# Optimization experiments

Measured on AMD Instinct MI355X. Metric: run time of the kernel, lower is better.

The kernel has to match this reference:

```python
import jax, jax.numpy as jnp
import numpy as np

E = 1024
H = 16
D = E // H  # head dim 64


def setup_inputs() -> dict:
    key = jax.random.key(0)
    ks = jax.random.split(key, 8)
    B, S = 4, 2048
    scale = 1.0 / np.sqrt(E)
    return {
        "Q": jax.random.normal(ks[0], (B, S, E), jnp.float32),
        "K": jax.random.normal(ks[1], (B, S, E), jnp.float32),
        "V": jax.random.normal(ks[2], (B, S, E), jnp.float32),
        "Wq": jax.random.normal(ks[3], (E, E), jnp.float32) * scale,
        "Wk": jax.random.normal(ks[4], (E, E), jnp.float32) * scale,
        "Wv": jax.random.normal(ks[5], (E, E), jnp.float32) * scale,
        "Wo": jax.random.normal(ks[6], (E, E), jnp.float32) * scale,
        "bo": jax.random.normal(ks[7], (E,), jnp.float32) * 0.01,
    }


def _split_heads(x):
    # [B, S, E] -> [B, H, S, D]
    B, S, _ = x.shape
    return x.reshape(B, S, H, D).transpose(0, 2, 1, 3)


def reference(Q, K, V, Wq, Wk, Wv, Wo, bo):
    # Linear (torch nn.Linear: x @ W.T), no bias for QKV
    q = _split_heads(Q @ Wq.T)  # [B,H,Sq,D]
    k = _split_heads(K @ Wk.T)  # [B,H,Sk,D]
    v = _split_heads(V @ Wv.T)  # [B,H,Sk,D]
    scores = jnp.einsum("bhqd,bhkd->bhqk", q, k)
    # NOTE: original code computes scores/sqrt(D) but applies softmax to the
    # UNSCALED scores (a bug we reproduce faithfully).
    attn = jax.nn.softmax(scores, axis=-1)
    out = jnp.einsum("bhqk,bhkd->bhqd", attn, v)  # [B,H,Sq,D]
    B, _, Sq, _ = out.shape
    out = out.transpose(0, 2, 1, 3).reshape(B, Sq, E)
    return out @ Wo.T + bo
```

## Files before the change

### kernel.cpp

```cpp
#include <hip/hip_runtime.h>
#include <hip/hip_bf16.h>


using bf16 = __hip_bfloat16;
typedef __attribute__((ext_vector_type(8))) short short8;
typedef __attribute__((ext_vector_type(4))) short short4v;
typedef _Float16 half8 __attribute__((ext_vector_type(8)));
typedef __attribute__((ext_vector_type(4))) float floatx4;

#define E_DIM 1024
#define H_NUM 16
#define D_DIM 64
#define B_NUM 4
#define S_LEN 2048
#define M_TOT 8192

__device__ __forceinline__ void async_ld16(const void* g, void* l) {
  __builtin_amdgcn_global_load_lds(
      (const __attribute__((address_space(1))) unsigned int*)g,
      (__attribute__((address_space(3))) unsigned int*)l, 16, 0, 0);
}

__device__ __forceinline__ short f2bf(float x) {
  unsigned u = __builtin_bit_cast(unsigned, x);
  u += 0x7FFFu + ((u >> 16) & 1u);
  return (short)(u >> 16);
}

__global__ void cvt_f32_bf16(const float* __restrict__ src,
                             short* __restrict__ dst, int n4) {
  int i = blockIdx.x * blockDim.x + threadIdx.x;
  if (i >= n4) return;
  float4 v = ((const float4*)src)[i];
  short4v o;
  o[0] = f2bf(v.x); o[1] = f2bf(v.y); o[2] = f2bf(v.z); o[3] = f2bf(v.w);
  ((short4v*)dst)[i] = o;
}

template <int OUT_MODE>
__global__ __launch_bounds__(256, 3) void gemm_k(
    const short* __restrict__ A, const short* __restrict__ Wb,
    const float* __restrict__ bias, void* __restrict__ Cp,
    int M, int N, int K) {
  __shared__ __align__(16) short As[128 * 32];
  __shared__ __align__(16) short Ws[128 * 32];
  const int tid = threadIdx.x;
  const int wave = tid >> 6;
  const int lane = tid & 63;
  const int quad = lane >> 4;
  const int l16 = lane & 15;
  const int wr = wave >> 1, wc = wave & 1;

  int mBase, nBase;
  {
    const int nwg = gridDim.x * gridDim.y;
    int l = blockIdx.x + gridDim.x * blockIdx.y;
    l = (l & 7) * (nwg >> 3) + (l >> 3);
    nBase = (l & 7) * 128;
    mBase = (l >> 3) * 128;
  }

  floatx4 acc[4][4] = {};

  const int sR = lane >> 2, sC = (lane & 3) * 8;
  for (int kb = 0; kb < K; kb += 32) {
    __syncthreads();
#pragma unroll
    for (int t = 0; t < 2; t++) {
      const int r0 = wave * 32 + t * 16;
      async_ld16(&Wb[(size_t)(nBase + r0 + sR) * K + kb + sC], &Ws[r0 * 32]);
    }
#pragma unroll
    for (int t = 0; t < 2; t++) {
      const int r0 = wave * 32 + t * 16;
      async_ld16(&A[(size_t)(mBase + r0 + sR) * K + kb + sC], &As[r0 * 32]);
    }
    __syncthreads();

    short8 af[4], wf[4];
#pragma unroll
    for (int i = 0; i < 4; i++)
      af[i] = *(const short8*)&As[(wr * 64 + i * 16 + l16) * 32 + quad * 8];
#pragma unroll
    for (int j = 0; j < 4; j++)
      wf[j] = *(const short8*)&Ws[(wc * 64 + j * 16 + l16) * 32 + quad * 8];
#pragma unroll
    for (int i = 0; i < 4; i++)
#pragma unroll
      for (int j = 0; j < 4; j++)
        acc[i][j] = __builtin_amdgcn_mfma_f32_16x16x32_bf16(af[i], wf[j], acc[i][j], 0, 0, 0);
  }

#pragma unroll
  for (int i = 0; i < 4; i++) {
    const int row0 = mBase + wr * 64 + i * 16 + quad * 4;
#pragma unroll
    for (int j = 0; j < 4; j++) {
      const int col = nBase + wc * 64 + j * 16 + l16;
      const float bv = (OUT_MODE == 2) ? bias[col] : 0.0f;
#pragma unroll
      for (int r = 0; r < 4; r++) {
        const float val = acc[i][j][r] + bv;
        if (OUT_MODE == 0)
          ((_Float16*)Cp)[(size_t)(row0 + r) * N + col] = (_Float16)val;
        else if (OUT_MODE == 1)
          ((short*)Cp)[(size_t)col * M + (row0 + r)] = f2bf(val);
        else
          ((float*)Cp)[(size_t)(row0 + r) * N + col] = val;
      }
    }
  }
}

__global__ __launch_bounds__(256, 3) void flash_attn(
    const _Float16* __restrict__ q, const _Float16* __restrict__ k,
    const short* __restrict__ vt, short* __restrict__ o) {
  __shared__ __align__(16) char smem[51200];
  short* Vts = (short*)smem;
  _Float16* Ks = (_Float16*)(smem + 16384);
  short* PsW = (short*)(smem + 16384 + (threadIdx.x >> 6) * 8704);

  const int tid = threadIdx.x;
  const int wave = tid >> 6;
  const int lane = tid & 63;
  const int quad = lane >> 4;
  const int l16 = lane & 15;

  int qRow0, h, b;
  {
    int l = blockIdx.x + ((blockIdx.y + (blockIdx.z << 4)) << 4);
    l = (l & 7) * 128 + (l >> 3);
    qRow0 = (l & 15) * 128;
    h = (l >> 4) & 15;
    b = l >> 8;
  }

  const _Float16* qp = q + (size_t)(b * S_LEN + qRow0) * E_DIM + h * D_DIM;
  const _Float16* kp = k + (size_t)(b * S_LEN) * E_DIM + h * D_DIM;
  const short* vtp = vt + (size_t)(h * D_DIM) * M_TOT + b * S_LEN;
  short* op = o + (size_t)(b * S_LEN + qRow0) * E_DIM + h * D_DIM;

  half8 qf[2][2];
#pragma unroll
  for (int i = 0; i < 2; i++)
#pragma unroll
    for (int ks = 0; ks < 2; ks++)
      qf[i][ks] = *(const half8*)&qp[(size_t)(wave * 32 + i * 16 + l16) * E_DIM + ks * 32 + quad * 8];

  short8 ones;
#pragma unroll
  for (int j = 0; j < 8; j++) ones[j] = (l16 == 0) ? (short)0x3F80 : (short)0;

  floatx4 oacc[2][4] = {};
  floatx4 oaccL[2] = {};

  const int kRow = lane >> 3, kChk = lane & 7;
  const int vRow = lane >> 4, vChk = lane & 15;

  for (int kt = 0; kt < 16; kt++) {
    __syncthreads();
#pragma unroll
    for (int t = 0; t < 4; t++) {
      const int r0 = wave * 32 + t * 8;
      const int gcol = (kChk ^ kRow) * 8;
      async_ld16(&kp[(size_t)(kt * 128 + r0 + kRow) * E_DIM + gcol], &Ks[r0 * 64]);
    }
#pragma unroll
    for (int t = 0; t < 4; t++) {
      const int r0 = wave * 16 + t * 4;
      const int row = r0 + vRow;
      const int gcol = (vChk ^ (row & 15)) * 8;
      async_ld16(&vtp[(size_t)row * M_TOT + kt * 128 + gcol], &Vts[r0 * 128]);
    }
    __syncthreads();

    floatx4 sc[2][8] = {};
    __builtin_amdgcn_s_setprio(1);
#pragma unroll
    for (int jt = 0; jt < 8; jt++) {
#pragma unroll
      for (int ks = 0; ks < 2; ks++) {
        const int scol = ((ks * 4 + quad) ^ (l16 & 7)) * 8;
        half8 kf = *(const half8*)&Ks[(jt * 16 + l16) * 64 + scol];
        sc[0][jt] = __builtin_amdgcn_mfma_f32_16x16x32_f16(qf[0][ks], kf, sc[0][jt], 0, 0, 0);
        sc[1][jt] = __builtin_amdgcn_mfma_f32_16x16x32_f16(qf[1][ks], kf, sc[1][jt], 0, 0, 0);
      }
    }
    __builtin_amdgcn_s_setprio(0);
    __syncthreads();

#pragma unroll
    for (int i = 0; i < 2; i++)
#pragma unroll
      for (int r = 0; r < 4; r++) {
        const int prow = i * 16 + quad * 4 + r;
#pragma unroll
        for (int jt = 0; jt < 8; jt++) {
          const float p = __expf(sc[i][jt][r] - 40.0f);
          PsW[prow * 136 + jt * 16 + l16] = f2bf(p);
        }
      }

    __builtin_amdgcn_s_setprio(1);
#pragma unroll
    for (int ks = 0; ks < 4; ks++) {
      short8 pf[2];
#pragma unroll
      for (int i = 0; i < 2; i++)
        pf[i] = *(const short8*)&PsW[(i * 16 + l16) * 136 + ks * 32 + quad * 8];
#pragma unroll
      for (int dt = 0; dt < 4; dt++) {
        const int scol = ((ks * 4 + quad) ^ l16) * 8;
        short8 vf = *(const short8*)&Vts[(dt * 16 + l16) * 128 + scol];
        oacc[0][dt] = __builtin_amdgcn_mfma_f32_16x16x32_bf16(pf[0], vf, oacc[0][dt], 0, 0, 0);
        oacc[1][dt] = __builtin_amdgcn_mfma_f32_16x16x32_bf16(pf[1], vf, oacc[1][dt], 0, 0, 0);
      }
      oaccL[0] = __builtin_amdgcn_mfma_f32_16x16x32_bf16(pf[0], ones, oaccL[0], 0, 0, 0);
      oaccL[1] = __builtin_amdgcn_mfma_f32_16x16x32_bf16(pf[1], ones, oaccL[1], 0, 0, 0);
    }
    __builtin_amdgcn_s_setprio(0);
  }

#pragma unroll
  for (int i = 0; i < 2; i++)
#pragma unroll
    for (int r = 0; r < 4; r++) {
      const float ls = __shfl(oaccL[i][r], lane & 48, 64);
      const float inv = 1.0f / ls;
      const int row = wave * 32 + i * 16 + quad * 4 + r;
#pragma unroll
      for (int dt = 0; dt < 4; dt++)
        op[(size_t)row * E_DIM + dt * 16 + l16] = f2bf(oacc[i][dt][r] * inv);
    }
}

extern "C" void kernel_launch(void* const* d_in, const int* in_sizes, int n_in,
                              void* d_out, int out_size, void* d_ws, size_t ws_size,
                              hipStream_t stream) {
  const float* Q  = (const float*)d_in[0];
  const float* K  = (const float*)d_in[1];
  const float* V  = (const float*)d_in[2];
  const float* Wq = (const float*)d_in[3];
  const float* Wk = (const float*)d_in[4];
  const float* Wv = (const float*)d_in[5];
  const float* Wo = (const float*)d_in[6];
  const float* bo = (const float*)d_in[7];
  float* out = (float*)d_out;

  char* ws = (char*)d_ws;
  const size_t wsz = (size_t)E_DIM * E_DIM * 2;
  short* wqb = (short*)ws; ws += wsz;
  short* wkb = (short*)ws; ws += wsz;
  short* wvb = (short*)ws; ws += wsz;
  short* wob = (short*)ws; ws += wsz;
  const size_t asz = (size_t)M_TOT * E_DIM * 2;
  _Float16* qw = (_Float16*)ws; ws += asz;
  _Float16* kw = (_Float16*)ws; ws += asz;
  short* vtw = (short*)ws;      ws += asz;
  short* aw  = (short*)ws;      ws += asz;
  short* abf = aw;

  dim3 blk(256);
  const int n4w = E_DIM * E_DIM / 4;
  cvt_f32_bf16<<<dim3(n4w / 256), blk, 0, stream>>>(Wq, wqb, n4w);
  cvt_f32_bf16<<<dim3(n4w / 256), blk, 0, stream>>>(Wk, wkb, n4w);
  cvt_f32_bf16<<<dim3(n4w / 256), blk, 0, stream>>>(Wv, wvb, n4w);
  cvt_f32_bf16<<<dim3(n4w / 256), blk, 0, stream>>>(Wo, wob, n4w);

  const int n4a = M_TOT * E_DIM / 4;
  dim3 ggrid(E_DIM / 128, M_TOT / 128);
  cvt_f32_bf16<<<dim3(n4a / 256), blk, 0, stream>>>(Q, abf, n4a);
  gemm_k<0><<<ggrid, blk, 0, stream>>>(abf, wqb, nullptr, qw, M_TOT, E_DIM, E_DIM);
  cvt_f32_bf16<<<dim3(n4a / 256), blk, 0, stream>>>(K, abf, n4a);
  gemm_k<0><<<ggrid, blk, 0, stream>>>(abf, wkb, nullptr, kw, M_TOT, E_DIM, E_DIM);
  cvt_f32_bf16<<<dim3(n4a / 256), blk, 0, stream>>>(V, abf, n4a);
  gemm_k<1><<<ggrid, blk, 0, stream>>>(abf, wvb, nullptr, vtw, M_TOT, E_DIM, E_DIM);
  flash_attn<<<dim3(S_LEN / 128, H_NUM, B_NUM), blk, 0, stream>>>(qw, kw, vtw, aw);
  gemm_k<2><<<ggrid, blk, 0, stream>>>(aw, wob, bo, out, M_TOT, E_DIM, E_DIM);
}
```

Measured before the change: 376.3 us.

## Batch QKV projections into one launch with swizzled BK64 tiles and LDS-staged transpose

Merges the four weight conversions and the three activation conversions into two batched kernels. The Q/K/V projections now run as a single grid-z batched GEMM, reusing the output buffer as scratch for the bf16 K and V copies. The GEMM now uses a K-step of 64 with an XOR-swizzled LDS layout to cut bank conflicts and halve barrier count. The transposed V output is staged through LDS so it can be written with coalesced 16-byte stores instead of strided scalar stores. This removes launch gaps and uncoalesced writes, at the cost of more LDS per block and a different block-to-tile mapping.

```diff
diff --git a/kernel.cpp b/kernel.cpp
--- a/kernel.cpp
+++ b/kernel.cpp
@@ -27,23 +27,46 @@
   return (short)(u >> 16);
 }
 
-__global__ void cvt_f32_bf16(const float* __restrict__ src,
-                             short* __restrict__ dst, int n4) {
-  int i = blockIdx.x * blockDim.x + threadIdx.x;
-  if (i >= n4) return;
+__global__ void cvt_w4(const float* __restrict__ a, const float* __restrict__ b,
+                       const float* __restrict__ c, const float* __restrict__ d,
+                       short* __restrict__ oa, short* __restrict__ ob,
+                       short* __restrict__ oc, short* __restrict__ od) {
+  const int z = blockIdx.y;
+  const float* src = z == 0 ? a : z == 1 ? b : z == 2 ? c : d;
+  short* dst = z == 0 ? oa : z == 1 ? ob : z == 2 ? oc : od;
+  const int i = blockIdx.x * blockDim.x + threadIdx.x;
   float4 v = ((const float4*)src)[i];
   short4v o;
   o[0] = f2bf(v.x); o[1] = f2bf(v.y); o[2] = f2bf(v.z); o[3] = f2bf(v.w);
   ((short4v*)dst)[i] = o;
 }
 
-template <int OUT_MODE>
+__global__ void cvt_a3(const float* __restrict__ a, const float* __restrict__ b,
+                       const float* __restrict__ c, short* __restrict__ oa,
+                       short* __restrict__ ob, short* __restrict__ oc) {
+  const int z = blockIdx.y;
+  const float* src = z == 0 ? a : z == 1 ? b : c;
+  short* dst = z == 0 ? oa : z == 1 ? ob : oc;
+  const int i = blockIdx.x * blockDim.x + threadIdx.x;
+  float4 v = ((const float4*)src)[i];
+  short4v o;
+  o[0] = f2bf(v.x); o[1] = f2bf(v.y); o[2] = f2bf(v.z); o[3] = f2bf(v.w);
+  ((short4v*)dst)[i] = o;
+}
+
+template <int MODE>
 __global__ __launch_bounds__(256, 3) void gemm_k(
-    const short* __restrict__ A, const short* __restrict__ Wb,
-    const float* __restrict__ bias, void* __restrict__ Cp,
-    int M, int N, int K) {
-  __shared__ __align__(16) short As[128 * 32];
-  __shared__ __align__(16) short Ws[128 * 32];
+    const short* __restrict__ A0, const short* __restrict__ A1,
+    const short* __restrict__ A2, const short* __restrict__ W0,
+    const short* __restrict__ W1, const short* __restrict__ W2,
+    void* __restrict__ C0, void* __restrict__ C1p, void* __restrict__ C2p,
+    const float* __restrict__ bias) {
+  __shared__ __align__(16) char smem[MODE == 0 ? 34816 : 32768];
+  short* As = (short*)smem;
+  short* Ws = (short*)(smem + 16384);
+  short* Cs = (short*)smem;
+
+  const int M = M_TOT, N = E_DIM, K = E_DIM;
   const int tid = threadIdx.x;
   const int wave = tid >> 6;
   const int lane = tid & 63;
@@ -51,63 +74,94 @@
   const int l16 = lane & 15;
   const int wr = wave >> 1, wc = wave & 1;
 
-  int mBase, nBase;
-  {
-    const int nwg = gridDim.x * gridDim.y;
-    int l = blockIdx.x + gridDim.x * blockIdx.y;
-    l = (l & 7) * (nwg >> 3) + (l >> 3);
-    nBase = (l & 7) * 128;
-    mBase = (l >> 3) * 128;
+  const int z = (MODE == 0) ? blockIdx.z : 0;
+  const short* A = (MODE == 0) ? (z == 0 ? A0 : z == 1 ? A1 : A2) : A0;
+  const short* W = (MODE == 0) ? (z == 0 ? W0 : z == 1 ? W1 : W2) : W0;
+
+  const int nBase = (blockIdx.y & 7) * 128;
+  const int mBase = (blockIdx.x * 8 + (blockIdx.y >> 3)) * 128;
+
+  const int sRow = lane >> 3;
+  const int sSwz = ((lane & 7) ^ sRow) * 8;
+  const int rdSwz0 = ((0 * 4 + quad) ^ (l16 & 7)) * 8;
+  const int rdSwz1 = ((1 * 4 + quad) ^ (l16 & 7)) * 8;
+
+  floatx4 acc[4][4] = {};
+
+  for (int kb = 0; kb < K; kb += 64) {
+    __syncthreads();
+#pragma unroll
+    for (int t = 0; t < 4; t++) {
+      const int r0 = wave * 32 + t * 8;
+      async_ld16(&W[(size_t)(nBase + r0 + sRow) * K + kb + sSwz], &Ws[r0 * 64]);
+      async_ld16(&A[(size_t)(mBase + r0 + sRow) * K + kb + sSwz], &As[r0 * 64]);
+    }
+    __syncthreads();
+#pragma unroll
+    for (int ks = 0; ks < 2; ks++) {
+      const int rs = ks ? rdSwz1 : rdSwz0;
+      short8 af[4], wf[4];
+#pragma unroll
+      for (int i = 0; i < 4; i++)
+        af[i] = *(const short8*)&As[(wr * 64 + i * 16 + l16) * 64 + rs];
+#pragma unroll
+      for (int j = 0; j < 4; j++)
+        wf[j] = *(const short8*)&Ws[(wc * 64 + j * 16 + l16) * 64 + rs];
+#pragma unroll
+      for (int i = 0; i < 4; i++)
+#pragma unroll
+        for (int j = 0; j < 4; j++)
+          acc[i][j] = __builtin_amdgcn_mfma_f32_16x16x32_bf16(af[i], wf[j], acc[i][j], 0, 0, 0);
+    }
   }
 
-  floatx4 acc[4][4] = {};
-
-  const int sR = lane >> 2, sC = (lane & 3) * 8;
-  for (int kb = 0; kb < K; kb += 32) {
-    __syncthreads();
-#pragma unroll
-    for (int t = 0; t < 2; t++) {
-      const int r0 = wave * 32 + t * 16;
-      async_ld16(&Wb[(size_t)(nBase + r0 + sR) * K + kb + sC], &Ws[r0 * 32]);
-    }
-#pragma unroll
-    for (int t = 0; t < 2; t++) {
-      const int r0 = wave * 32 + t * 16;
-      async_ld16(&A[(size_t)(mBase + r0 + sR) * K + kb + sC], &As[r0 * 32]);
-    }
-    __syncthreads();
-
-    short8 af[4], wf[4];
-#pragma unroll
-    for (int i = 0; i < 4; i++)
-      af[i] = *(const short8*)&As[(wr * 64 + i * 16 + l16) * 32 + quad * 8];
-#pragma unroll
-    for (int j = 0; j < 4; j++)
-      wf[j] = *(const short8*)&Ws[(wc * 64 + j * 16 + l16) * 32 + quad * 8];
-#pragma unroll
-    for (int i = 0; i < 4; i++)
-#pragma unroll
-      for (int j = 0; j < 4; j++)
-        acc[i][j] = __builtin_amdgcn_mfma_f32_16x16x32_bf16(af[i], wf[j], acc[i][j], 0, 0, 0);
-  }
-
-#pragma unroll
-  for (int i = 0; i < 4; i++) {
-    const int row0 = mBase + wr * 64 + i * 16 + quad * 4;
-#pragma unroll
-    for (int j = 0; j < 4; j++) {
-      const int col = nBase + wc * 64 + j * 16 + l16;
-      const float bv = (OUT_MODE == 2) ? bias[col] : 0.0f;
-#pragma unroll
-      for (int r = 0; r < 4; r++) {
-        const float val = acc[i][j][r] + bv;
-        if (OUT_MODE == 0)
-          ((_Float16*)Cp)[(size_t)(row0 + r) * N + col] = (_Float16)val;
-        else if (OUT_MODE == 1)
-          ((short*)Cp)[(size_t)col * M + (row0 + r)] = f2bf(val);
-        else
-          ((float*)Cp)[(size_t)(row0 + r) * N + col] = val;
-      }
+  if (MODE == 2) {
+#pragma unroll
+    for (int i = 0; i < 4; i++) {
+      const int row0 = mBase + wr * 64 + i * 16 + quad * 4;
+#pragma unroll
+      for (int j = 0; j < 4; j++) {
+        const int col = nBase + wc * 64 + j * 16 + l16;
+        const float bv = bias[col];
+#pragma unroll
+        for (int r = 0; r < 4; r++)
+          ((float*)C0)[(size_t)(row0 + r) * N + col] = acc[i][j][r] + bv;
+      }
+    }
+  } else if (z != 2) {
+    _Float16* C = (_Float16*)(z == 0 ? C0 : C1p);
+#pragma unroll
+    for (int i = 0; i < 4; i++) {
+      const int row0 = mBase + wr * 64 + i * 16 + quad * 4;
+#pragma unroll
+      for (int j = 0; j < 4; j++) {
+        const int col = nBase + wc * 64 + j * 16 + l16;
+#pragma unroll
+        for (int r = 0; r < 4; r++)
+          C[(size_t)(row0 + r) * N + col] = (_Float16)acc[i][j][r];
+      }
+    }
+  } else {
+    __syncthreads();
+#pragma unroll
+    for (int i = 0; i < 4; i++) {
+      const int rl = wr * 64 + i * 16 + quad * 4;
+#pragma unroll
+      for (int j = 0; j < 4; j++) {
+        const int cl = wc * 64 + j * 16 + l16;
+#pragma unroll
+        for (int r = 0; r < 4; r++)
+          Cs[cl * 136 + rl + r] = f2bf(acc[i][j][r]);
+      }
+    }
+    __syncthreads();
+    short* C = (short*)C2p;
+#pragma unroll
+    for (int p = 0; p < 8; p++) {
+      const int id = p * 256 + tid;
+      const int nl = id >> 4, mc = (id & 15) * 8;
+      *(short8*)&C[(size_t)(nBase + nl) * M + mBase + mc] =
+          *(const short8*)&Cs[nl * 136 + mc];
     }
   }
 }
@@ -258,23 +312,19 @@
   _Float16* kw = (_Float16*)ws; ws += asz;
   short* vtw = (short*)ws;      ws += asz;
   short* aw  = (short*)ws;      ws += asz;
-  short* abf = aw;
+  short* qbf = aw;
+  short* kbf = (short*)d_out;
+  short* vbf = (short*)d_out + (size_t)M_TOT * E_DIM;
 
   dim3 blk(256);
-  const int n4w = E_DIM * E_DIM / 4;
-  cvt_f32_bf16<<<dim3(n4w / 256), blk, 0, stream>>>(Wq, wqb, n4w);
-  cvt_f32_bf16<<<dim3(n4w / 256), blk, 0, stream>>>(Wk, wkb, n4w);
-  cvt_f32_bf16<<<dim3(n4w / 256), blk, 0, stream>>>(Wv, wvb, n4w);
-  cvt_f32_bf16<<<dim3(n4w / 256), blk, 0, stream>>>(Wo, wob, n4w);
-
-  const int n4a = M_TOT * E_DIM / 4;
-  dim3 ggrid(E_DIM / 128, M_TOT / 128);
-  cvt_f32_bf16<<<dim3(n4a / 256), blk, 0, stream>>>(Q, abf, n4a);
-  gemm_k<0><<<ggrid, blk, 0, stream>>>(abf, wqb, nullptr, qw, M_TOT, E_DIM, E_DIM);
-  cvt_f32_bf16<<<dim3(n4a / 256), blk, 0, stream>>>(K, abf, n4a);
-  gemm_k<0><<<ggrid, blk, 0, stream>>>(abf, wkb, nullptr, kw, M_TOT, E_DIM, E_DIM);
-  cvt_f32_bf16<<<dim3(n4a / 256), blk, 0, stream>>>(V, abf, n4a);
-  gemm_k<1><<<ggrid, blk, 0, stream>>>(abf, wvb, nullptr, vtw, M_TOT, E_DIM, E_DIM);
+  cvt_w4<<<dim3(E_DIM * E_DIM / 4 / 256, 4), blk, 0, stream>>>(
+      Wq, Wk, Wv, Wo, wqb, wkb, wvb, wob);
+  cvt_a3<<<dim3(M_TOT * E_DIM / 4 / 256, 3), blk, 0, stream>>>(
+      Q, K, V, qbf, kbf, vbf);
+
+  gemm_k<0><<<dim3(8, 64, 3), blk, 0, stream>>>(
+      qbf, kbf, vbf, wqb, wkb, wvb, qw, kw, vtw, nullptr);
   flash_attn<<<dim3(S_LEN / 128, H_NUM, B_NUM), blk, 0, stream>>>(qw, kw, vtw, aw);
-  gemm_k<2><<<ggrid, blk, 0, stream>>>(aw, wob, bo, out, M_TOT, E_DIM, E_DIM);
-}
+  gemm_k<2><<<dim3(8, 64, 1), blk, 0, stream>>>(
+      aw, nullptr, nullptr, wob, nullptr, nullptr, out, nullptr, nullptr, bo);
+}
```

New measurement: 331.7 us. 1.13x faster.
